# Optimization experiments

Measured on AMD Instinct MI355X. Metric: run time of the kernel, lower is better.

The kernel has to match this reference:

```python
import jax, jax.numpy as jnp
import numpy as np
import math

B, T, C, H = 4, 2048, 1024, 16

def setup_inputs() -> dict:
    key = jax.random.key(0)
    ks = jax.random.split(key, 9)
    s = 0.02
    return {
        "x":  jax.random.normal(ks[0], (B, T, C), dtype=jnp.float32),
        "Wq": jax.random.normal(ks[1], (C, C), dtype=jnp.float32) * s,
        "bq": jax.random.normal(ks[2], (C,), dtype=jnp.float32) * s,
        "Wk": jax.random.normal(ks[3], (C, C), dtype=jnp.float32) * s,
        "bk": jax.random.normal(ks[4], (C,), dtype=jnp.float32) * s,
        "Wv": jax.random.normal(ks[5], (C, C), dtype=jnp.float32) * s,
        "bv": jax.random.normal(ks[6], (C,), dtype=jnp.float32) * s,
        "Wp": jax.random.normal(ks[7], (C, C), dtype=jnp.float32) * s,
        "bp": jax.random.normal(ks[8], (C,), dtype=jnp.float32) * s,
    }

def reference(x, Wq, bq, Wk, bk, Wv, bv, Wp, bp):
    b, t, c = x.shape
    h = H
    d = c // h
    # torch Linear: y = x @ W.T + b
    q = (x @ Wq.T + bq).reshape(b, t, h, d).transpose(0, 2, 1, 3)  # [B,H,T,d]
    k = (x @ Wk.T + bk).reshape(b, t, h, d).transpose(0, 2, 1, 3)
    v = (x @ Wv.T + bv).reshape(b, t, h, d).transpose(0, 2, 1, 3)
    att = jnp.einsum('bhqd,bhkd->bhqk', q, k) * (1.0 / math.sqrt(d))  # [B,H,T,T]
    causal = jnp.tril(jnp.ones((t, t), dtype=bool))
    att = jnp.where(causal[None, None, :, :], att, -jnp.inf)
    att = jax.nn.softmax(att, axis=-1)
    # attn_drop / resid_drop are identity in eval mode
    y = jnp.einsum('bhqk,bhkd->bhqd', att, v)        # [B,H,T,d]
    y = y.transpose(0, 2, 1, 3).reshape(b, t, c)      # [B,T,C]
    y = y @ Wp.T + bp
    return y
```

## Files before the change

### kernel.cpp

```cpp
#include <hip/hip_runtime.h>
#include <hip/hip_bf16.h>

typedef __attribute__((ext_vector_type(8))) short bf16x8;
typedef __attribute__((ext_vector_type(4))) float f32x4;

struct bf16x8_s { __hip_bfloat16 h[8]; };
struct bf16x4_s { __hip_bfloat16 h[4]; };

#if defined(__has_builtin)
#if __has_builtin(__builtin_amdgcn_exp2f)
#define EXP2F(x) __builtin_amdgcn_exp2f(x)
#endif
#endif
#ifndef EXP2F
#define EXP2F(x) exp2f(x)
#endif

__global__ void cvt_kernel(const float* __restrict__ in,
                           __hip_bfloat16* __restrict__ out, int n8) {
  int i = blockIdx.x * blockDim.x + threadIdx.x;
  if (i >= n8) return;
  const float4* p = reinterpret_cast<const float4*>(in) + (size_t)i * 2;
  float4 a = p[0], b = p[1];
  bf16x8_s o;
  o.h[0] = __float2bfloat16(a.x); o.h[1] = __float2bfloat16(a.y);
  o.h[2] = __float2bfloat16(a.z); o.h[3] = __float2bfloat16(a.w);
  o.h[4] = __float2bfloat16(b.x); o.h[5] = __float2bfloat16(b.y);
  o.h[6] = __float2bfloat16(b.z); o.h[7] = __float2bfloat16(b.w);
  *reinterpret_cast<bf16x8_s*>(out + (size_t)i * 8) = o;
}

__global__ void cvt4_kernel(const float* __restrict__ w0,
                            const float* __restrict__ w1,
                            const float* __restrict__ w2,
                            const float* __restrict__ w3,
                            __hip_bfloat16* __restrict__ out) {
  const int bid = blockIdx.x;
  const int seg = bid >> 9;
  const int i = (bid & 511) * 256 + threadIdx.x;
  const float* src = seg == 0 ? w0 : seg == 1 ? w1 : seg == 2 ? w2 : w3;
  const float4* p = reinterpret_cast<const float4*>(src) + (size_t)i * 2;
  float4 a = p[0], b = p[1];
  bf16x8_s o;
  o.h[0] = __float2bfloat16(a.x); o.h[1] = __float2bfloat16(a.y);
  o.h[2] = __float2bfloat16(a.z); o.h[3] = __float2bfloat16(a.w);
  o.h[4] = __float2bfloat16(b.x); o.h[5] = __float2bfloat16(b.y);
  o.h[6] = __float2bfloat16(b.z); o.h[7] = __float2bfloat16(b.w);
  *reinterpret_cast<bf16x8_s*>(out + (size_t)seg * 1048576 + (size_t)i * 8) = o;
}

__device__ __forceinline__ void stage_tile(const __hip_bfloat16* src,
                                           char* lds, int tid) {
#pragma unroll
  for (int s = 0; s < 4; ++s) {
    const int c = s * 256 + tid;
    const int row = c >> 3;
    const int cb = (((c & 7) << 4) ^ ((row & 7) << 4));
    __builtin_amdgcn_global_load_lds(
        (const __attribute__((address_space(1))) void*)((const char*)(src + (size_t)row * 1024) + cb),
        (__attribute__((address_space(3))) void*)(lds + s * 4096 + (tid & 192) * 16),
        16, 0, 0);
  }
}

template <int MODE>
__global__ __launch_bounds__(256) void gemm128(
    const __hip_bfloat16* __restrict__ A, const __hip_bfloat16* __restrict__ W,
    const float* __restrict__ b0, const float* __restrict__ b1,
    const float* __restrict__ b2, void* __restrict__ O0,
    void* __restrict__ O1, void* __restrict__ O2) {
  constexpr float SC = 0.18033688011112042f;
  __shared__ char smem[32768];
  const int tid = threadIdx.x;
  const int lane = tid & 63;
  const int lrow = lane & 15;
  const int lhi = lane >> 4;
  const int wid = tid >> 6;
  const int wm = wid >> 1, wn = wid & 1;
  const int xr = (lrow & 7) << 4;

  const int n = blockIdx.x;
  const int wg = MODE == 0 ? (n & 7) * 192 + (n >> 3) : (n & 7) * 64 + (n >> 3);
  const int tm = wg & 63;
  const int tn = wg >> 6;
  const int row0 = tm * 128;

  const __hip_bfloat16* Ap = A + (size_t)row0 * 1024;
  const __hip_bfloat16* Wp = W + (size_t)(tn * 128) * 1024;

  f32x4 acc[4][4] = {};

  for (int k0 = 0; k0 < 1024; k0 += 64) {
    stage_tile(Ap + k0, smem, tid);
    stage_tile(Wp + k0, smem + 16384, tid);
    __syncthreads();
    bf16x8 af[4][2], bfr[4][2];
#pragma unroll
    for (int m = 0; m < 4; ++m) {
      const int ar = wm * 64 + m * 16 + lrow;
#pragma unroll
      for (int kk = 0; kk < 2; ++kk)
        af[m][kk] = *reinterpret_cast<const bf16x8*>(
            smem + ar * 128 + ((kk * 64 + lhi * 16) ^ xr));
    }
#pragma unroll
    for (int nn = 0; nn < 4; ++nn) {
      const int br = wn * 64 + nn * 16 + lrow;
#pragma unroll
      for (int kk = 0; kk < 2; ++kk)
        bfr[nn][kk] = *reinterpret_cast<const bf16x8*>(
            smem + 16384 + br * 128 + ((kk * 64 + lhi * 16) ^ xr));
    }
    __builtin_amdgcn_s_setprio(1);
#pragma unroll
    for (int kk = 0; kk < 2; ++kk)
#pragma unroll
      for (int m = 0; m < 4; ++m)
#pragma unroll
        for (int nn = 0; nn < 4; ++nn)
          acc[m][nn] = __builtin_amdgcn_mfma_f32_16x16x32_bf16(
              af[m][kk], bfr[nn][kk], acc[m][nn], 0, 0, 0);
    __builtin_amdgcn_s_setprio(0);
    __syncthreads();
  }

  char* epi = smem + wid * 8192;
  const int grow0 = row0 + wm * 64;

  if constexpr (MODE == 0) {
    const int sel = tn >> 3;
    const int cloc = (tn & 7) * 128 + wn * 64;
    const float* bias = sel == 0 ? b0 : sel == 1 ? b1 : b2;
    float bv4[4];
#pragma unroll
    for (int nn = 0; nn < 4; ++nn) bv4[nn] = bias[cloc + nn * 16 + lrow];

    if (sel != 2) {
      __hip_bfloat16* dst = sel == 0 ? (__hip_bfloat16*)O0 : (__hip_bfloat16*)O1;
#pragma unroll
      for (int mg = 0; mg < 4; ++mg) {
#pragma unroll
        for (int nn = 0; nn < 4; ++nn)
#pragma unroll
          for (int i = 0; i < 4; ++i) {
            float v = acc[mg][nn][i] + bv4[nn];
            if (sel == 0) v *= SC;
            ((__hip_bfloat16*)epi)[(lhi * 4 + i) * 72 + nn * 16 + lrow] =
                __float2bfloat16(v);
          }
#pragma unroll
        for (int ps = 0; ps < 2; ++ps) {
          const int r = ps * 8 + (lane >> 3);
          bf16x8 val = *reinterpret_cast<const bf16x8*>(epi + r * 144 + (lane & 7) * 16);
          const int grow = grow0 + mg * 16 + r;
          *reinterpret_cast<bf16x8*>(&dst[(size_t)grow * 1024 + cloc + (lane & 7) * 8]) = val;
        }
      }
    } else {
      __hip_bfloat16* dst = (__hip_bfloat16*)O2;
      const int h = cloc >> 6;
      const int bb = grow0 >> 11;
      const int t0 = grow0 & 2047;
      __hip_bfloat16* vb = dst + ((size_t)(bb * 16 + h) * 64) * 2048;
#pragma unroll
      for (int ng = 0; ng < 4; ++ng) {
#pragma unroll
        for (int m = 0; m < 4; ++m)
#pragma unroll
          for (int i = 0; i < 4; ++i) {
            const float v = acc[m][ng][i] + bv4[ng];
            ((__hip_bfloat16*)epi)[lrow * 72 + m * 16 + lhi * 4 + i] =
                __float2bfloat16(v);
          }
#pragma unroll
        for (int ps = 0; ps < 2; ++ps) {
          const int dr = ps * 8 + (lane >> 3);
          bf16x8 val = *reinterpret_cast<const bf16x8*>(epi + dr * 144 + (lane & 7) * 16);
          const int d = ng * 16 + dr;
          *reinterpret_cast<bf16x8*>(&vb[(size_t)d * 2048 + t0 + (lane & 7) * 8]) = val;
        }
      }
    }
  } else {
    float* dst = (float*)O0;
    const int cloc = tn * 128 + wn * 64;
    float bv4[4];
#pragma unroll
    for (int nn = 0; nn < 4; ++nn) bv4[nn] = b0[cloc + nn * 16 + lrow];
#pragma unroll
    for (int mg = 0; mg < 4; ++mg) {
#pragma unroll
      for (int nn = 0; nn < 4; ++nn)
#pragma unroll
        for (int i = 0; i < 4; ++i)
          ((float*)epi)[(lhi * 4 + i) * 68 + nn * 16 + lrow] =
              acc[mg][nn][i] + bv4[nn];
#pragma unroll
      for (int ps = 0; ps < 4; ++ps) {
        const int r = ps * 4 + (lane >> 4);
        float4 val = *reinterpret_cast<const float4*>(epi + r * 272 + (lane & 15) * 16);
        const int grow = grow0 + mg * 16 + r;
        *reinterpret_cast<float4*>(&dst[(size_t)grow * 1024 + cloc + (lane & 15) * 4]) = val;
      }
    }
  }
}

__device__ __forceinline__ void stage_kv(char* __restrict__ smem, int buf,
                                         const __hip_bfloat16* __restrict__ Kb,
                                         const __hip_bfloat16* __restrict__ Vb,
                                         int kv0, int tid) {
  const int w = tid >> 6, l = tid & 63;
  char* base = smem + buf * 16384;
#pragma unroll
  for (int s = 0; s < 2; ++s) {
    const int c = s * 256 + w * 64 + l;
    const int row = c >> 3;
    const int scb = ((c & 7) << 4) ^ ((row & 7) << 4);
    __builtin_amdgcn_global_load_lds(
        (const __attribute__((address_space(1))) void*)(Kb + (size_t)(kv0 + row) * 1024 + (scb >> 1)),
        (__attribute__((address_space(3))) void*)(base + s * 4096 + w * 1024), 16, 0, 0);
  }
#pragma unroll
  for (int s = 0; s < 2; ++s) {
    const int c = s * 256 + w * 64 + l;
    const int row = c >> 3;
    const int scb = ((c & 7) << 4) ^ ((row & 7) << 4);
    __builtin_amdgcn_global_load_lds(
        (const __attribute__((address_space(1))) void*)(Vb + (size_t)row * 2048 + kv0 + (scb >> 1)),
        (__attribute__((address_space(3))) void*)(base + 8192 + s * 4096 + w * 1024), 16, 0, 0);
  }
}

template <bool MASKED>
__device__ __forceinline__ void attn_step(
    int kv0, int q0w, int lrow, int lhi, const char* __restrict__ kvb,
    const bf16x8 qf[2][2], f32x4 o[2][4], float m[2], float l[2],
    __hip_bfloat16* __restrict__ P) {
  constexpr float TH = 8.0f;
  const int xr = (lrow & 7) << 4;
  f32x4 s[2][4] = {};
  __builtin_amdgcn_s_setprio(1);
#pragma unroll
  for (int g = 0; g < 4; ++g) {
    const char* rowp = kvb + (g * 16 + lrow) * 128;
#pragma unroll
    for (int kk = 0; kk < 2; ++kk) {
      bf16x8 kf = *reinterpret_cast<const bf16x8*>(rowp + ((kk * 64 + lhi * 16) ^ xr));
#pragma unroll
      for (int j = 0; j < 2; ++j)
        s[j][g] = __builtin_amdgcn_mfma_f32_16x16x32_bf16(kf, qf[j][kk], s[j][g], 0, 0, 0);
    }
  }
  __builtin_amdgcn_s_setprio(0);
  float mx[2];
#pragma unroll
  for (int j = 0; j < 2; ++j) {
    if (MASKED) {
#pragma unroll
      for (int g = 0; g < 4; ++g)
#pragma unroll
        for (int i = 0; i < 4; ++i) {
          const int k = kv0 + g * 16 + lhi * 4 + i;
          if (k > q0w + j * 16 + lrow) s[j][g][i] = -1e30f;
        }
    }
    float gm[4];
#pragma unroll
    for (int g = 0; g < 4; ++g)
      gm[g] = fmaxf(fmaxf(s[j][g][0], s[j][g][1]), fmaxf(s[j][g][2], s[j][g][3]));
    float t = fmaxf(fmaxf(gm[0], gm[1]), fmaxf(gm[2], gm[3]));
    t = fmaxf(t, __shfl_xor(t, 16));
    t = fmaxf(t, __shfl_xor(t, 32));
    mx[j] = t;
  }
  const int need = (mx[0] > m[0] + TH) || (mx[1] > m[1] + TH);
  if (__any(need)) {
#pragma unroll
    for (int j = 0; j < 2; ++j) {
      const float nm = fmaxf(m[j], mx[j]);
      const float al = EXP2F(m[j] - nm);
      m[j] = nm;
      l[j] *= al;
      float a4[4];
#pragma unroll
      for (int i = 0; i < 4; ++i) a4[i] = __shfl(al, 4 * lhi + i, 16);
#pragma unroll
      for (int f = 0; f < 4; ++f)
#pragma unroll
        for (int i = 0; i < 4; ++i) o[j][f][i] *= a4[i];
    }
  }
#pragma unroll
  for (int j = 0; j < 2; ++j) {
    float gs[4];
#pragma unroll
    for (int g = 0; g < 4; ++g) {
      bf16x4_s t4;
      float p0 = EXP2F(s[j][g][0] - m[j]);
      float p1 = EXP2F(s[j][g][1] - m[j]);
      float p2 = EXP2F(s[j][g][2] - m[j]);
      float p3 = EXP2F(s[j][g][3] - m[j]);
      t4.h[0] = __float2bfloat16(p0); t4.h[1] = __float2bfloat16(p1);
      t4.h[2] = __float2bfloat16(p2); t4.h[3] = __float2bfloat16(p3);
      gs[g] = (p0 + p1) + (p2 + p3);
      *reinterpret_cast<bf16x4_s*>(P + (j * 16 + lrow) * 72 + g * 16 + lhi * 4) = t4;
    }
    float sum = (gs[0] + gs[1]) + (gs[2] + gs[3]);
    sum += __shfl_xor(sum, 16);
    sum += __shfl_xor(sum, 32);
    l[j] += sum;
  }
  bf16x8 pf[2][2];
#pragma unroll
  for (int j = 0; j < 2; ++j)
#pragma unroll
    for (int n = 0; n < 2; ++n)
      pf[j][n] = *reinterpret_cast<const bf16x8*>(P + (j * 16 + lrow) * 72 + n * 32 + lhi * 8);
  __builtin_amdgcn_s_setprio(1);
#pragma unroll
  for (int n = 0; n < 2; ++n)
#pragma unroll
    for (int f = 0; f < 4; ++f) {
      bf16x8 vf = *reinterpret_cast<const bf16x8*>(
          kvb + 8192 + (f * 16 + lrow) * 128 + ((n * 64 + lhi * 16) ^ xr));
#pragma unroll
      for (int j = 0; j < 2; ++j)
        o[j][f] = __builtin_amdgcn_mfma_f32_16x16x32_bf16(pf[j][n], vf, o[j][f], 0, 0, 0);
    }
  __builtin_amdgcn_s_setprio(0);
}

__global__ __launch_bounds__(256, 2) void attn_fwd(
    const __hip_bfloat16* __restrict__ Q, const __hip_bfloat16* __restrict__ Km,
    const __hip_bfloat16* __restrict__ Vt, __hip_bfloat16* __restrict__ Y) {
  constexpr int T = 2048, C = 1024, D = 64;
  const int tid = threadIdx.x;
  const int wid = tid >> 6;
  const int lane = tid & 63;
  const int lrow = lane & 15;
  const int lhi = lane >> 4;
  const int n = blockIdx.x;
  const int xcd = n & 7;
  const int w8 = n >> 3;
  const int bh = xcd * 8 + (w8 & 7);
  const int pr = w8 >> 3;
  const int qtA = 15 - pr;
  const int qtB = pr;
  const int b = bh >> 4, h = bh & 15;
  const int q0A = qtA * 128 + wid * 32;
  const int q0B = qtB * 128 + wid * 32;

  const __hip_bfloat16* Qb = Q + ((size_t)b * T) * C + h * D;
  const __hip_bfloat16* Kb = Km + ((size_t)b * T) * C + h * D;
  const __hip_bfloat16* Vb = Vt + (size_t)bh * D * T;

  __shared__ char smem[51200];
  __hip_bfloat16* P = (__hip_bfloat16*)(smem + 32768 + wid * 4608);

  bf16x8 qfA[2][2], qfB[2][2];
#pragma unroll
  for (int j = 0; j < 2; ++j)
#pragma unroll
    for (int kk = 0; kk < 2; ++kk) {
      qfA[j][kk] = *reinterpret_cast<const bf16x8*>(
          Qb + (size_t)(q0A + j * 16 + lrow) * C + kk * 32 + lhi * 8);
      qfB[j][kk] = *reinterpret_cast<const bf16x8*>(
          Qb + (size_t)(q0B + j * 16 + lrow) * C + kk * 32 + lhi * 8);
    }

  f32x4 oA[2][4] = {}, oB[2][4] = {};
  float mA[2] = {-1e30f, -1e30f}, lA[2] = {0.f, 0.f};
  float mB[2] = {-1e30f, -1e30f}, lB[2] = {0.f, 0.f};

  const int nt = 2 * qtA + 2;
  const int nsA = (q0A >> 6) + 1;
  const int nsB = (q0B >> 6) + 1;

  stage_kv(smem, 0, Kb, Vb, 0, tid);
  for (int t = 0; t < nt; ++t) {
    __syncthreads();
    if (t + 1 < nt) stage_kv(smem, (t + 1) & 1, Kb, Vb, (t + 1) * 64, tid);
    const char* kvb = smem + (t & 1) * 16384;
    if (t < nsA) {
      if (t == nsA - 1)
        attn_step<true>(t * 64, q0A, lrow, lhi, kvb, qfA, oA, mA, lA, P);
      else
        attn_step<false>(t * 64, q0A, lrow, lhi, kvb, qfA, oA, mA, lA, P);
    }
    if (t < nsB) {
      if (t == nsB - 1)
        attn_step<true>(t * 64, q0B, lrow, lhi, kvb, qfB, oB, mB, lB, P);
      else
        attn_step<false>(t * 64, q0B, lrow, lhi, kvb, qfB, oB, mB, lB, P);
    }
  }

#pragma unroll
  for (int j = 0; j < 2; ++j) {
    float l4[4];
#pragma unroll
    for (int i = 0; i < 4; ++i) l4[i] = __shfl(lA[j], 4 * lhi + i, 16);
#pragma unroll
    for (int f = 0; f < 4; ++f)
#pragma unroll
      for (int i = 0; i < 4; ++i) {
        const int row = q0A + j * 16 + 4 * lhi + i;
        Y[((size_t)b * T + row) * C + h * D + f * 16 + lrow] =
            __float2bfloat16(oA[j][f][i] / l4[i]);
      }
  }
#pragma unroll
  for (int j = 0; j < 2; ++j) {
    float l4[4];
#pragma unroll
    for (int i = 0; i < 4; ++i) l4[i] = __shfl(lB[j], 4 * lhi + i, 16);
#pragma unroll
    for (int f = 0; f < 4; ++f)
#pragma unroll
      for (int i = 0; i < 4; ++i) {
        const int row = q0B + j * 16 + 4 * lhi + i;
        Y[((size_t)b * T + row) * C + h * D + f * 16 + lrow] =
            __float2bfloat16(oB[j][f][i] / l4[i]);
      }
  }
}

extern "C" void kernel_launch(void* const* d_in, const int* in_sizes, int n_in,
                              void* d_out, int out_size, void* d_ws,
                              size_t ws_size, hipStream_t stream) {
  const float* x = (const float*)d_in[0];
  const float* Wq = (const float*)d_in[1];
  const float* bq = (const float*)d_in[2];
  const float* Wk = (const float*)d_in[3];
  const float* bk = (const float*)d_in[4];
  const float* Wv = (const float*)d_in[5];
  const float* bv = (const float*)d_in[6];
  const float* Wp = (const float*)d_in[7];
  const float* bp = (const float*)d_in[8];
  float* out = (float*)d_out;

  __hip_bfloat16* ws = (__hip_bfloat16*)d_ws;
  __hip_bfloat16* xb = ws;
  __hip_bfloat16* wqb = xb + 8388608;
  __hip_bfloat16* wpb = wqb + 3 * 1048576;
  __hip_bfloat16* Qs = wqb + 4 * 1048576;
  __hip_bfloat16* Ks = Qs + 8388608;
  __hip_bfloat16* Vts = Ks + 8388608;
  __hip_bfloat16* Ys = Vts + 8388608;

  cvt_kernel<<<4096, 256, 0, stream>>>(x, xb, 1048576);
  cvt4_kernel<<<2048, 256, 0, stream>>>(Wq, Wk, Wv, Wp, wqb);

  gemm128<0><<<dim3(1536), 256, 0, stream>>>(xb, wqb, bq, bk, bv, Qs, Ks, Vts);

  attn_fwd<<<dim3(512), 256, 0, stream>>>(Qs, Ks, Vts, Ys);

  gemm128<1><<<dim3(512), 256, 0, stream>>>(Ys, wpb, bp, nullptr, nullptr, out,
                                            nullptr, nullptr);
}
```

Measured before the change: 178.5 us.

## Interleave both query tiles per KV step and replace syncthreads with explicit vmcnt waits

The two per-wave query tiles (A and B) are now handled in one combined step. Each K/V fragment read from LDS feeds the MFMAs for both tiles, which raises instruction-level parallelism and halves LDS fragment reads. `__syncthreads` is replaced by a raw s_barrier plus an explicit `s_waitcnt vmcnt(4)`, so the next tile's async global-to-LDS loads can stay in flight while the current tile computes. The hardware exp2 builtin is swapped for plain `exp2f`. The costs are higher register pressure from holding both score tiles under `launch_bounds(256,2)`, possible spills, and reliance on hand-placed waitcnts being correct.

Result: slower. 193.2 us (+8.2%).

```diff
diff --git a/kernel.cpp b/kernel.cpp
--- a/kernel.cpp
+++ b/kernel.cpp
@@ -6,15 +6,6 @@
 
 struct bf16x8_s { __hip_bfloat16 h[8]; };
 struct bf16x4_s { __hip_bfloat16 h[4]; };
-
-#if defined(__has_builtin)
-#if __has_builtin(__builtin_amdgcn_exp2f)
-#define EXP2F(x) __builtin_amdgcn_exp2f(x)
-#endif
-#endif
-#ifndef EXP2F
-#define EXP2F(x) exp2f(x)
-#endif
 
 __global__ void cvt_kernel(const float* __restrict__ in,
                            __hip_bfloat16* __restrict__ out, int n8) {
@@ -232,31 +223,14 @@
   }
 }
 
-template <bool MASKED>
-__device__ __forceinline__ void attn_step(
-    int kv0, int q0w, int lrow, int lhi, const char* __restrict__ kvb,
-    const bf16x8 qf[2][2], f32x4 o[2][4], float m[2], float l[2],
-    __hip_bfloat16* __restrict__ P) {
+__device__ __forceinline__ void softmax_tile(
+    f32x4 s[2][4], bool masked, int kv0, int q0w, int lrow, int lhi,
+    f32x4 o[2][4], float m[2], float l[2], __hip_bfloat16* __restrict__ P,
+    bf16x8 pf[2][2]) {
   constexpr float TH = 8.0f;
-  const int xr = (lrow & 7) << 4;
-  f32x4 s[2][4] = {};
-  __builtin_amdgcn_s_setprio(1);
-#pragma unroll
-  for (int g = 0; g < 4; ++g) {
-    const char* rowp = kvb + (g * 16 + lrow) * 128;
-#pragma unroll
-    for (int kk = 0; kk < 2; ++kk) {
-      bf16x8 kf = *reinterpret_cast<const bf16x8*>(rowp + ((kk * 64 + lhi * 16) ^ xr));
-#pragma unroll
-      for (int j = 0; j < 2; ++j)
-        s[j][g] = __builtin_amdgcn_mfma_f32_16x16x32_bf16(kf, qf[j][kk], s[j][g], 0, 0, 0);
-    }
-  }
-  __builtin_amdgcn_s_setprio(0);
-  float mx[2];
-#pragma unroll
-  for (int j = 0; j < 2; ++j) {
-    if (MASKED) {
+  if (masked) {
+#pragma unroll
+    for (int j = 0; j < 2; ++j)
 #pragma unroll
       for (int g = 0; g < 4; ++g)
 #pragma unroll
@@ -264,7 +238,10 @@
           const int k = kv0 + g * 16 + lhi * 4 + i;
           if (k > q0w + j * 16 + lrow) s[j][g][i] = -1e30f;
         }
-    }
+  }
+  float mx[2];
+#pragma unroll
+  for (int j = 0; j < 2; ++j) {
     float gm[4];
 #pragma unroll
     for (int g = 0; g < 4; ++g)
@@ -279,7 +256,7 @@
 #pragma unroll
     for (int j = 0; j < 2; ++j) {
       const float nm = fmaxf(m[j], mx[j]);
-      const float al = EXP2F(m[j] - nm);
+      const float al = exp2f(m[j] - nm);
       m[j] = nm;
       l[j] *= al;
       float a4[4];
@@ -297,10 +274,10 @@
 #pragma unroll
     for (int g = 0; g < 4; ++g) {
       bf16x4_s t4;
-      float p0 = EXP2F(s[j][g][0] - m[j]);
-      float p1 = EXP2F(s[j][g][1] - m[j]);
-      float p2 = EXP2F(s[j][g][2] - m[j]);
-      float p3 = EXP2F(s[j][g][3] - m[j]);
+      float p0 = exp2f(s[j][g][0] - m[j]);
+      float p1 = exp2f(s[j][g][1] - m[j]);
+      float p2 = exp2f(s[j][g][2] - m[j]);
+      float p3 = exp2f(s[j][g][3] - m[j]);
       t4.h[0] = __float2bfloat16(p0); t4.h[1] = __float2bfloat16(p1);
       t4.h[2] = __float2bfloat16(p2); t4.h[3] = __float2bfloat16(p3);
       gs[g] = (p0 + p1) + (p2 + p3);
@@ -310,23 +287,53 @@
     sum += __shfl_xor(sum, 16);
     sum += __shfl_xor(sum, 32);
     l[j] += sum;
-  }
-  bf16x8 pf[2][2];
-#pragma unroll
-  for (int j = 0; j < 2; ++j)
-#pragma unroll
-    for (int n = 0; n < 2; ++n)
-      pf[j][n] = *reinterpret_cast<const bf16x8*>(P + (j * 16 + lrow) * 72 + n * 32 + lhi * 8);
+#pragma unroll
+    for (int nn = 0; nn < 2; ++nn)
+      pf[j][nn] = *reinterpret_cast<const bf16x8*>(
+          P + (j * 16 + lrow) * 72 + nn * 32 + lhi * 8);
+  }
+}
+
+template <bool DOB>
+__device__ __forceinline__ void attn_step2(
+    int kv0, int q0A, int q0B, bool mA, bool mB, int lrow, int lhi,
+    const char* __restrict__ kvb, const bf16x8 qfA[2][2],
+    const bf16x8 qfB[2][2], f32x4 oA[2][4], f32x4 oB[2][4], float mAr[2],
+    float lAr[2], float mBr[2], float lBr[2], __hip_bfloat16* __restrict__ P) {
+  const int xr = (lrow & 7) << 4;
+  f32x4 sA[2][4] = {}, sB[2][4] = {};
   __builtin_amdgcn_s_setprio(1);
 #pragma unroll
-  for (int n = 0; n < 2; ++n)
+  for (int g = 0; g < 4; ++g) {
+    const char* rowp = kvb + (g * 16 + lrow) * 128;
+#pragma unroll
+    for (int kk = 0; kk < 2; ++kk) {
+      bf16x8 kf = *reinterpret_cast<const bf16x8*>(rowp + ((kk * 64 + lhi * 16) ^ xr));
+      sA[0][g] = __builtin_amdgcn_mfma_f32_16x16x32_bf16(kf, qfA[0][kk], sA[0][g], 0, 0, 0);
+      sA[1][g] = __builtin_amdgcn_mfma_f32_16x16x32_bf16(kf, qfA[1][kk], sA[1][g], 0, 0, 0);
+      if (DOB) {
+        sB[0][g] = __builtin_amdgcn_mfma_f32_16x16x32_bf16(kf, qfB[0][kk], sB[0][g], 0, 0, 0);
+        sB[1][g] = __builtin_amdgcn_mfma_f32_16x16x32_bf16(kf, qfB[1][kk], sB[1][g], 0, 0, 0);
+      }
+    }
+  }
+  __builtin_amdgcn_s_setprio(0);
+  bf16x8 pfA[2][2], pfB[2][2];
+  softmax_tile(sA, mA, kv0, q0A, lrow, lhi, oA, mAr, lAr, P, pfA);
+  if (DOB) softmax_tile(sB, mB, kv0, q0B, lrow, lhi, oB, mBr, lBr, P, pfB);
+  __builtin_amdgcn_s_setprio(1);
+#pragma unroll
+  for (int nn = 0; nn < 2; ++nn)
 #pragma unroll
     for (int f = 0; f < 4; ++f) {
       bf16x8 vf = *reinterpret_cast<const bf16x8*>(
-          kvb + 8192 + (f * 16 + lrow) * 128 + ((n * 64 + lhi * 16) ^ xr));
-#pragma unroll
-      for (int j = 0; j < 2; ++j)
-        o[j][f] = __builtin_amdgcn_mfma_f32_16x16x32_bf16(pf[j][n], vf, o[j][f], 0, 0, 0);
+          kvb + 8192 + (f * 16 + lrow) * 128 + ((nn * 64 + lhi * 16) ^ xr));
+      oA[0][f] = __builtin_amdgcn_mfma_f32_16x16x32_bf16(pfA[0][nn], vf, oA[0][f], 0, 0, 0);
+      oA[1][f] = __builtin_amdgcn_mfma_f32_16x16x32_bf16(pfA[1][nn], vf, oA[1][f], 0, 0, 0);
+      if (DOB) {
+        oB[0][f] = __builtin_amdgcn_mfma_f32_16x16x32_bf16(pfB[0][nn], vf, oB[0][f], 0, 0, 0);
+        oB[1][f] = __builtin_amdgcn_mfma_f32_16x16x32_bf16(pfB[1][nn], vf, oB[1][f], 0, 0, 0);
+      }
     }
   __builtin_amdgcn_s_setprio(0);
 }
@@ -379,20 +386,24 @@
 
   stage_kv(smem, 0, Kb, Vb, 0, tid);
   for (int t = 0; t < nt; ++t) {
-    __syncthreads();
-    if (t + 1 < nt) stage_kv(smem, (t + 1) & 1, Kb, Vb, (t + 1) * 64, tid);
+    __builtin_amdgcn_s_barrier();
+    __builtin_amdgcn_sched_barrier(0);
+    if (t + 1 < nt) {
+      stage_kv(smem, (t + 1) & 1, Kb, Vb, (t + 1) * 64, tid);
+      asm volatile("s_waitcnt vmcnt(4)" ::: "memory");
+    } else {
+      asm volatile("s_waitcnt vmcnt(0)" ::: "memory");
+    }
+    __builtin_amdgcn_sched_barrier(0);
     const char* kvb = smem + (t & 1) * 16384;
     if (t < nsA) {
-      if (t == nsA - 1)
-        attn_step<true>(t * 64, q0A, lrow, lhi, kvb, qfA, oA, mA, lA, P);
+      const bool mAq = (t == nsA - 1);
+      if (t < nsB)
+        attn_step2<true>(t * 64, q0A, q0B, mAq, t == nsB - 1, lrow, lhi, kvb,
+                         qfA, qfB, oA, oB, mA, lA, mB, lB, P);
       else
-        attn_step<false>(t * 64, q0A, lrow, lhi, kvb, qfA, oA, mA, lA, P);
-    }
-    if (t < nsB) {
-      if (t == nsB - 1)
-        attn_step<true>(t * 64, q0B, lrow, lhi, kvb, qfB, oB, mB, lB, P);
-      else
-        attn_step<false>(t * 64, q0B, lrow, lhi, kvb, qfB, oB, mB, lB, P);
+        attn_step2<false>(t * 64, q0A, q0B, mAq, false, lrow, lhi, kvb, qfA,
+                          qfB, oA, oB, mA, lA, mB, lB, P);
     }
   }
 
```
